# Performance work log

Hardware: AMD Instinct MI355X
Metric: run time of the kernel (lower is better)

## Reference

```python
import jax, jax.numpy as jnp
import numpy as np

EMBED_DIM = 32
PIC_RES = 96
KERNEL_BW = 3.0
STEP_SIZE = 0.5
NB_ITERS = 3


def setup_inputs() -> dict:
    key = jax.random.key(0)
    # scale down so exp(bw * x^T x) stays in a safe numeric range
    x_in = jax.random.normal(key, (1, EMBED_DIM, PIC_RES, PIC_RES), dtype=jnp.float32) * 0.1
    return {"x_in": x_in}


def reference(x_in):
    # x: [D, N], N = res*res pixels
    x = x_in.reshape(EMBED_DIM, -1)
    outs = []
    for _ in range(NB_ITERS):
        # affinity K[i,j] = exp(bw * <x_i, x_j>), shape [N, N]
        K = jnp.exp(KERNEL_BW * (x.T @ x))
        # column sums d_j = sum_i K[i,j] (== torch diag(K^T @ 1)); K is symmetric
        d = K.sum(axis=0)
        # x <- x @ (step * K diag(1/d) + (1-step) I)
        x = STEP_SIZE * (x @ K) / d + (1.0 - STEP_SIZE) * x
        outs.append(x.reshape(EMBED_DIM, PIC_RES, PIC_RES))
    final = x.reshape(EMBED_DIM, PIC_RES, PIC_RES)
    return final, jnp.stack(outs)
```

## Files before the change

kernel.cpp:

```cpp
#include <hip/hip_runtime.h>
#include <hip/hip_bf16.h>
#include <math.h>


#define D 32
#define NPIX 9216
#define NSPLIT 12
#define JB 128
#define NJB (NPIX / JB)
#define IPB (NPIX / NSPLIT)
#define ICH 64
#define NCH (IPB / ICH)
#define TS  40

typedef __attribute__((ext_vector_type(8))) short short8;
typedef __attribute__((ext_vector_type(4))) short short4v;
typedef __attribute__((ext_vector_type(4))) float f32x4;

#if __has_builtin(__builtin_amdgcn_exp2f)
#define EXP2F __builtin_amdgcn_exp2f
#else
#define EXP2F exp2f
#endif

#define SQC3 2.08040504f

__device__ __forceinline__ unsigned pack2_bf16(float a, float b) {
    union { __hip_bfloat162 h2; unsigned u; } c;
    c.h2 = __float22bfloat162_rn(make_float2(a, b));
    return c.u;
}
__device__ __forceinline__ short pack1_bf16(float a) {
    union { __hip_bfloat16 h; unsigned short s; } c;
    c.h = __float2bfloat16(a);
    return (short)c.s;
}

__device__ __forceinline__ void gll16(const void* g, void* l) {
    __builtin_amdgcn_global_load_lds(
        (const __attribute__((address_space(1))) void*)g,
        (__attribute__((address_space(3))) void*)l, 16, 0, 0);
}

__global__ __launch_bounds__(256, 4) void accum_kernel(
    const short* __restrict__ xb,
    const short* __restrict__ xbT,
    float* __restrict__ num_part,
    float* __restrict__ den_part)
{
    __shared__ __align__(16) short sT[3][2048];
    __shared__ __align__(16) short sV[3][2048];

    const int t = threadIdx.x;
    const int wid = t >> 6, lane = t & 63, quad = lane >> 4, m = lane & 15;
    const int bj = blockIdx.x % NJB, bi = blockIdx.x / NJB;
    const int j0 = bj * JB + wid * 32;
    const int i0b = bi * IPB;

    short8 bfrag[2];
#pragma unroll
    for (int jt = 0; jt < 2; ++jt)
        bfrag[jt] = *(const short8*)&xbT[(size_t)(j0 + jt * 16 + m) * D + quad * 8];

    short8 ones;
#pragma unroll
    for (int e = 0; e < 8; ++e) ones[e] = (short)0x3F80;

    f32x4 acc[2][2] = {};
    f32x4 accden[2] = {};

    const int ch = t >> 7, cq = (t >> 5) & 3, ci = t & 31;
    const int invi = (((ci >> 3) & 1) << 4) | (((ci >> 2) & 1) << 3)
                   | (((ci >> 4) & 1) << 2) | (ci & 3);
    const short* srcT = xbT + (size_t)(i0b + ch * 32 + invi) * D + cq * 8;
    const short* srcV = xb + (size_t)ci * NPIX + i0b + ch * 32 + cq * 8;
    short* dT = &sT[0][0] + wid * 512;
    short* dV = &sV[0][0] + wid * 512;

    gll16(srcT, dT);
    gll16(srcV, dV);
    gll16(srcT + (size_t)ICH * D, dT + 2048);
    gll16(srcV + ICH,             dV + 2048);

#pragma unroll
    for (int n = 0; n < NCH; ++n) {
        if (n + 1 < NCH) asm volatile("s_waitcnt vmcnt(2)" ::: "memory");
        else             asm volatile("s_waitcnt vmcnt(0)" ::: "memory");
        __builtin_amdgcn_s_barrier();
        __builtin_amdgcn_sched_barrier(0);

        if (n + 2 < NCH) {
            gll16(srcT + (size_t)(n + 2) * (ICH * D), dT + ((n + 2) % 3) * 2048);
            gll16(srcV + (n + 2) * ICH,               dV + ((n + 2) % 3) * 2048);
        }

        const short* bT = &sT[n % 3][0];
        const short* bV = &sV[n % 3][0];
#pragma unroll
        for (int h = 0; h < 2; ++h) {
            const int rb = (h * 128 + quad * 32 + m) * 8;
            short8 aT0 = *(const short8*)&bT[rb];
            short8 aT1 = *(const short8*)&bT[rb + 128];
            short8 aV0 = *(const short8*)&bV[rb];
            short8 aV1 = *(const short8*)&bV[rb + 128];

#pragma unroll
            for (int jt = 0; jt < 2; ++jt) {
                f32x4 z = {0.f, 0.f, 0.f, 0.f};
                f32x4 s0 = __builtin_amdgcn_mfma_f32_16x16x32_bf16(aT0, bfrag[jt], z, 0, 0, 0);
                f32x4 s1 = __builtin_amdgcn_mfma_f32_16x16x32_bf16(aT1, bfrag[jt], z, 0, 0, 0);

                float w[8];
#pragma unroll
                for (int r = 0; r < 4; ++r) { w[r]     = EXP2F(s0[r]);
                                              w[4 + r] = EXP2F(s1[r]); }

                union { short8 s; unsigned u[4]; } wb;
                wb.u[0] = pack2_bf16(w[0], w[1]);
                wb.u[1] = pack2_bf16(w[2], w[3]);
                wb.u[2] = pack2_bf16(w[4], w[5]);
                wb.u[3] = pack2_bf16(w[6], w[7]);

                accden[jt] = __builtin_amdgcn_mfma_f32_16x16x32_bf16(ones, wb.s, accden[jt], 0, 0, 0);
                acc[0][jt] = __builtin_amdgcn_mfma_f32_16x16x32_bf16(aV0, wb.s, acc[0][jt], 0, 0, 0);
                acc[1][jt] = __builtin_amdgcn_mfma_f32_16x16x32_bf16(aV1, wb.s, acc[1][jt], 0, 0, 0);
            }
        }
    }

    float* np = num_part + (size_t)bi * D * NPIX;
#pragma unroll
    for (int dt = 0; dt < 2; ++dt)
#pragma unroll
        for (int jt = 0; jt < 2; ++jt)
#pragma unroll
            for (int r = 0; r < 4; ++r)
                np[(dt * 16 + quad * 4 + r) * NPIX + j0 + jt * 16 + m] = acc[dt][jt][r];
#pragma unroll
    for (int jt = 0; jt < 2; ++jt)
        if (quad == 0) den_part[bi * NPIX + j0 + jt * 16 + m] = accden[jt][0];
}

__global__ __launch_bounds__(256) void combine_kernel(
    const float* __restrict__ xin,
    const float* __restrict__ num_part, const float* __restrict__ den_part,
    float* __restrict__ xout, float* __restrict__ xfinal,
    short* __restrict__ xb, short* __restrict__ xbT, int do_ms)
{
    __shared__ __align__(16) short tile[32 * TS];
    const int t = threadIdx.x;
    const int il = t & 31, q = t >> 5;
    const int i = blockIdx.x * 32 + il;
    const int d0 = q * 4;

    float inv = 0.f;
    if (do_ms) {
        float den = 0.f;
#pragma unroll
        for (int s = 0; s < NSPLIT; ++s) den += den_part[s * NPIX + i];
        inv = 0.5f / den;
    }

#pragma unroll
    for (int dd = 0; dd < 4; ++dd) {
        const int d = d0 + dd;
        const int idx = d * NPIX + i;
        float v;
        if (do_ms) {
            float nm = 0.f;
#pragma unroll
            for (int s = 0; s < NSPLIT; ++s) nm += num_part[(s * D + d) * NPIX + i];
            v = nm * inv + 0.5f * xin[idx];
            xout[idx] = v;
            if (xfinal) xfinal[idx] = v;
        } else {
            v = xin[idx];
        }
        xb[idx] = pack1_bf16(v);
        tile[il * TS + d] = pack1_bf16(v * SQC3);
    }
    __syncthreads();
    const int i2 = t >> 3, dc = (t & 7) * 4;
    *(short4v*)&xbT[(blockIdx.x * 32 + i2) * D + dc] =
        *(const short4v*)&tile[i2 * TS + dc];
}

extern "C" void kernel_launch(void* const* d_in, const int* in_sizes, int n_in,
                              void* d_out, int out_size, void* d_ws, size_t ws_size,
                              hipStream_t stream)
{
    const float* x0 = (const float*)d_in[0];
    float* out = (float*)d_out;
    const size_t slot = (size_t)D * NPIX;

    float* num_part = (float*)d_ws;
    float* den_part = num_part + (size_t)NSPLIT * slot;
    short* xb  = (short*)(den_part + (size_t)NSPLIT * NPIX);
    short* xbT = xb + slot;

    combine_kernel<<<dim3(NPIX / 32), dim3(256), 0, stream>>>(
        x0, nullptr, nullptr, nullptr, nullptr, xb, xbT, 0);

    for (int t = 0; t < 3; ++t) {
        accum_kernel<<<dim3(NJB * NSPLIT), dim3(256), 0, stream>>>(
            xb, xbT, num_part, den_part);
        const float* xin = (t == 0) ? x0 : (out + (size_t)t * slot);
        combine_kernel<<<dim3(NPIX / 32), dim3(256), 0, stream>>>(
            xin, num_part, den_part, out + (size_t)(t + 1) * slot,
            (t == 2) ? out : nullptr, xb, xbT, 1);
    }
}
```

Measured before the change: 151.1 us.

## Widen accum blocks to 512 threads so each staged chunk feeds twice the columns

Doubles the j-columns per block (JB 128→256) with 512 threads and 8 waves sharing each LDS-staged i-chunk. This halves the number of blocks and halves global-to-LDS traffic per unit of work. The global-load-to-LDS copies are split so half the threads load the transposed tile and half load the value tile, one load each per chunk. The main loop is also unrolled by three so the triple-buffer indices become compile-time constants. In exchange the grid is smaller, which may reduce the number of blocks resident per CU, and barriers now synchronise eight waves instead of four.

```diff
diff --git a/kernel.cpp b/kernel.cpp
--- a/kernel.cpp
+++ b/kernel.cpp
@@ -6,7 +6,7 @@
 #define D 32
 #define NPIX 9216
 #define NSPLIT 12
-#define JB 128
+#define JB 256
 #define NJB (NPIX / JB)
 #define IPB (NPIX / NSPLIT)
 #define ICH 64
@@ -36,13 +36,49 @@
     return (short)c.s;
 }
 
-__device__ __forceinline__ void gll16(const void* g, void* l) {
+__device__ __forceinline__ void gll16(const short* g, short* l) {
     __builtin_amdgcn_global_load_lds(
         (const __attribute__((address_space(1))) void*)g,
         (__attribute__((address_space(3))) void*)l, 16, 0, 0);
 }
 
-__global__ __launch_bounds__(256, 4) void accum_kernel(
+__device__ __forceinline__ void chunk_compute(
+    const short* bT, const short* bV, const short8* bfrag, const short8 ones,
+    f32x4 acc[2][2], f32x4 accden[2], int quad, int m)
+{
+#pragma unroll
+    for (int h = 0; h < 2; ++h) {
+        const int rb = (h * 128 + quad * 32 + m) * 8;
+        short8 aT0 = *(const short8*)&bT[rb];
+        short8 aT1 = *(const short8*)&bT[rb + 128];
+        short8 aV0 = *(const short8*)&bV[rb];
+        short8 aV1 = *(const short8*)&bV[rb + 128];
+
+#pragma unroll
+        for (int jt = 0; jt < 2; ++jt) {
+            f32x4 z = {0.f, 0.f, 0.f, 0.f};
+            f32x4 s0 = __builtin_amdgcn_mfma_f32_16x16x32_bf16(aT0, bfrag[jt], z, 0, 0, 0);
+            f32x4 s1 = __builtin_amdgcn_mfma_f32_16x16x32_bf16(aT1, bfrag[jt], z, 0, 0, 0);
+
+            float w[8];
+#pragma unroll
+            for (int r = 0; r < 4; ++r) { w[r]     = EXP2F(s0[r]);
+                                          w[4 + r] = EXP2F(s1[r]); }
+
+            union { short8 s; unsigned u[4]; } wb;
+            wb.u[0] = pack2_bf16(w[0], w[1]);
+            wb.u[1] = pack2_bf16(w[2], w[3]);
+            wb.u[2] = pack2_bf16(w[4], w[5]);
+            wb.u[3] = pack2_bf16(w[6], w[7]);
+
+            accden[jt] = __builtin_amdgcn_mfma_f32_16x16x32_bf16(ones, wb.s, accden[jt], 0, 0, 0);
+            acc[0][jt] = __builtin_amdgcn_mfma_f32_16x16x32_bf16(aV0, wb.s, acc[0][jt], 0, 0, 0);
+            acc[1][jt] = __builtin_amdgcn_mfma_f32_16x16x32_bf16(aV1, wb.s, acc[1][jt], 0, 0, 0);
+        }
+    }
+}
+
+__global__ __launch_bounds__(512, 4) void accum_kernel(
     const short* __restrict__ xb,
     const short* __restrict__ xbT,
     float* __restrict__ num_part,
@@ -69,64 +105,41 @@
     f32x4 acc[2][2] = {};
     f32x4 accden[2] = {};
 
-    const int ch = t >> 7, cq = (t >> 5) & 3, ci = t & 31;
+    const bool isT = (t < 256);
+    const int c = t & 255;
+    const int ch = c >> 7, cq = (c >> 5) & 3, ci = c & 31;
     const int invi = (((ci >> 3) & 1) << 4) | (((ci >> 2) & 1) << 3)
                    | (((ci >> 4) & 1) << 2) | (ci & 3);
-    const short* srcT = xbT + (size_t)(i0b + ch * 32 + invi) * D + cq * 8;
-    const short* srcV = xb + (size_t)ci * NPIX + i0b + ch * 32 + cq * 8;
-    short* dT = &sT[0][0] + wid * 512;
-    short* dV = &sV[0][0] + wid * 512;
-
-    gll16(srcT, dT);
-    gll16(srcV, dV);
-    gll16(srcT + (size_t)ICH * D, dT + 2048);
-    gll16(srcV + ICH,             dV + 2048);
-
-#pragma unroll
-    for (int n = 0; n < NCH; ++n) {
-        if (n + 1 < NCH) asm volatile("s_waitcnt vmcnt(2)" ::: "memory");
-        else             asm volatile("s_waitcnt vmcnt(0)" ::: "memory");
-        __builtin_amdgcn_s_barrier();
-        __builtin_amdgcn_sched_barrier(0);
-
-        if (n + 2 < NCH) {
-            gll16(srcT + (size_t)(n + 2) * (ICH * D), dT + ((n + 2) % 3) * 2048);
-            gll16(srcV + (n + 2) * ICH,               dV + ((n + 2) % 3) * 2048);
-        }
-
-        const short* bT = &sT[n % 3][0];
-        const short* bV = &sV[n % 3][0];
-#pragma unroll
-        for (int h = 0; h < 2; ++h) {
-            const int rb = (h * 128 + quad * 32 + m) * 8;
-            short8 aT0 = *(const short8*)&bT[rb];
-            short8 aT1 = *(const short8*)&bT[rb + 128];
-            short8 aV0 = *(const short8*)&bV[rb];
-            short8 aV1 = *(const short8*)&bV[rb + 128];
-
-#pragma unroll
-            for (int jt = 0; jt < 2; ++jt) {
-                f32x4 z = {0.f, 0.f, 0.f, 0.f};
-                f32x4 s0 = __builtin_amdgcn_mfma_f32_16x16x32_bf16(aT0, bfrag[jt], z, 0, 0, 0);
-                f32x4 s1 = __builtin_amdgcn_mfma_f32_16x16x32_bf16(aT1, bfrag[jt], z, 0, 0, 0);
-
-                float w[8];
-#pragma unroll
-                for (int r = 0; r < 4; ++r) { w[r]     = EXP2F(s0[r]);
-                                              w[4 + r] = EXP2F(s1[r]); }
-
-                union { short8 s; unsigned u[4]; } wb;
-                wb.u[0] = pack2_bf16(w[0], w[1]);
-                wb.u[1] = pack2_bf16(w[2], w[3]);
-                wb.u[2] = pack2_bf16(w[4], w[5]);
-                wb.u[3] = pack2_bf16(w[6], w[7]);
-
-                accden[jt] = __builtin_amdgcn_mfma_f32_16x16x32_bf16(ones, wb.s, accden[jt], 0, 0, 0);
-                acc[0][jt] = __builtin_amdgcn_mfma_f32_16x16x32_bf16(aV0, wb.s, acc[0][jt], 0, 0, 0);
-                acc[1][jt] = __builtin_amdgcn_mfma_f32_16x16x32_bf16(aV1, wb.s, acc[1][jt], 0, 0, 0);
-            }
-        }
-    }
+    const short* src0 = isT
+        ? xbT + (size_t)(i0b + ch * 32 + invi) * D + cq * 8
+        : xb + (size_t)ci * NPIX + i0b + ch * 32 + cq * 8;
+    const size_t srcStep = isT ? (size_t)ICH * D : (size_t)ICH;
+    short* dst = (isT ? &sT[0][0] : &sV[0][0]) + (wid & 3) * 512;
+
+    gll16(src0, dst);
+    gll16(src0 + srcStep, dst + 2048);
+    const short* psrc = src0 + 2 * srcStep;
+
+#define CHUNK(n, k)                                                          \
+    {                                                                        \
+        if ((n) + 1 < NCH) asm volatile("s_waitcnt vmcnt(1)" ::: "memory");  \
+        else               asm volatile("s_waitcnt vmcnt(0)" ::: "memory");  \
+        __builtin_amdgcn_s_barrier();                                        \
+        __builtin_amdgcn_sched_barrier(0);                                   \
+        if ((n) + 2 < NCH) {                                                 \
+            gll16(psrc, dst + (((k) + 2) % 3) * 2048);                       \
+            psrc += srcStep;                                                 \
+        }                                                                    \
+        chunk_compute(&sT[(k)][0], &sV[(k)][0], bfrag, ones, acc, accden,    \
+                      quad, m);                                              \
+    }
+
+    for (int g = 0; g < NCH / 3; ++g) {
+        CHUNK(3 * g + 0, 0)
+        CHUNK(3 * g + 1, 1)
+        CHUNK(3 * g + 2, 2)
+    }
+#undef CHUNK
 
     float* np = num_part + (size_t)bi * D * NPIX;
 #pragma unroll
@@ -202,7 +215,7 @@
         x0, nullptr, nullptr, nullptr, nullptr, xb, xbT, 0);
 
     for (int t = 0; t < 3; ++t) {
-        accum_kernel<<<dim3(NJB * NSPLIT), dim3(256), 0, stream>>>(
+        accum_kernel<<<dim3(NJB * NSPLIT), dim3(512), 0, stream>>>(
             xb, xbT, num_part, den_part);
         const float* xin = (t == 0) ? x0 : (out + (size_t)t * slot);
         combine_kernel<<<dim3(NPIX / 32), dim3(256), 0, stream>>>(
```

Measured after the change: 148.1 us. -2.0%, faster.
